# Performance work log

Hardware: AMD Instinct MI355X
Metric: run time of the kernel (lower is better)

## Reference

```python
import jax, jax.numpy as jnp
import numpy as np

N_NODES = 50000
N_EDGES = 800000
IN_DIM, HID, OUT = 512, 96, 64


def gcn_conv(x, W, b, src, dst, n_nodes):
    # PyG GCNConv: h = x W; aggregate with sym-normalized adjacency incl. self-loops; add bias.
    h = x @ W  # [N, out]
    ones = jnp.ones_like(dst, dtype=h.dtype)
    deg = jax.ops.segment_sum(ones, dst, num_segments=n_nodes) + 1.0  # +1 for self-loop
    dinv = jax.lax.rsqrt(deg)
    norm = dinv[src] * dinv[dst]  # [E]
    agg = jax.ops.segment_sum(h[src] * norm[:, None], dst, num_segments=n_nodes)
    agg = agg + h * (dinv * dinv)[:, None]  # self-loop messages
    return agg + b


def setup_inputs() -> dict:
    key = jax.random.key(0)
    ks = jax.random.split(key, 12)
    s = 0.05
    x = jax.random.normal(ks[0], (N_NODES, IN_DIM), jnp.float32)
    edge_index = jax.random.randint(ks[1], (2, N_EDGES), 0, N_NODES)
    return {
        "x": x,
        "edge_index": edge_index,
        "W0": jax.random.normal(ks[2], (IN_DIM, HID), jnp.float32) * s,
        "b0": jnp.zeros((HID,), jnp.float32),
        "W1": jax.random.normal(ks[3], (HID, HID), jnp.float32) * s,
        "b1": jnp.zeros((HID,), jnp.float32),
        "W2": jax.random.normal(ks[4], (HID, HID), jnp.float32) * s,
        "b2": jnp.zeros((HID,), jnp.float32),
        "fcW": jax.random.normal(ks[5], (HID, OUT), jnp.float32) * s,
        "fcb": jnp.zeros((OUT,), jnp.float32),
    }


def reference(x, edge_index, W0, b0, W1, b1, W2, b2, fcW, fcb):
    src, dst = edge_index[0], edge_index[1]
    n = x.shape[0]
    # eval mode: dropout is identity; bn=False so no batchnorm
    h = jax.nn.relu(gcn_conv(x, W0, b0, src, dst, n))
    h = jax.nn.relu(gcn_conv(h, W1, b1, src, dst, n))
    h = jax.nn.relu(gcn_conv(h, W2, b2, src, dst, n))
    out = h @ fcW + fcb
    return jnp.squeeze(out)
```

## Files before the change

kernel.cpp:

```cpp
#include <hip/hip_runtime.h>


constexpr int NN   = 50000;
constexpr int NE   = 800000;
constexpr int KIN  = 512;
constexpr int HIDD = 96;
constexpr int ODIM = 64;
constexpr int NBLK = (NN + 255) / 256;

typedef short bf16x8 __attribute__((ext_vector_type(8)));
typedef short s8v    __attribute__((ext_vector_type(8)));
typedef float f32x4  __attribute__((ext_vector_type(4)));
typedef _Float16 h8  __attribute__((ext_vector_type(8)));

__device__ inline short f2bf(float f) {
    union { float f; unsigned u; } v; v.f = f;
    unsigned r = v.u + 0x7FFFu + ((v.u >> 16) & 1u);
    return (short)(r >> 16);
}
__device__ inline short f2bf_trunc(float f) {
    union { float f; unsigned u; } v; v.f = f;
    return (short)(v.u >> 16);
}
__device__ inline float bf2f(short h) {
    union { unsigned u; float f; } v; v.u = ((unsigned)(unsigned short)h) << 16;
    return v.f;
}

__global__ void zero_int_kernel(int* __restrict__ p, int n) {
    int i = blockIdx.x * blockDim.x + threadIdx.x;
    if (i < n) p[i] = 0;
}

__global__ void hist_kernel(const int* __restrict__ dst, int* __restrict__ deg) {
    int e = blockIdx.x * blockDim.x + threadIdx.x;
    if (e < NE) atomicAdd(&deg[dst[e]], 1);
}

__global__ void scan1_kernel(const int* __restrict__ deg, int* __restrict__ excl,
                             int* __restrict__ partials) {
    __shared__ int tmp[256];
    const int tid = threadIdx.x;
    const int i = blockIdx.x * 256 + tid;
    const int v = (i < NN) ? deg[i] : 0;
    tmp[tid] = v;
    __syncthreads();
#pragma unroll
    for (int off = 1; off < 256; off <<= 1) {
        int t = (tid >= off) ? tmp[tid - off] : 0;
        __syncthreads();
        tmp[tid] += t;
        __syncthreads();
    }
    if (i < NN) excl[i] = tmp[tid] - v;
    if (tid == 255) partials[blockIdx.x] = tmp[tid];
}

__global__ void scan3_kernel(const int* __restrict__ excl, const int* __restrict__ partials,
                             const int* __restrict__ deg, int* __restrict__ rowstart,
                             float* __restrict__ dinv, int* __restrict__ cursor) {
    __shared__ int tmp[256];
    const int tid = threadIdx.x;
    tmp[tid] = (tid < (int)blockIdx.x) ? partials[tid] : 0;
    __syncthreads();
#pragma unroll
    for (int off = 128; off > 0; off >>= 1) {
        if (tid < off) tmp[tid] += tmp[tid + off];
        __syncthreads();
    }
    const int boff = tmp[0];
    const int i = blockIdx.x * 256 + tid;
    if (i < NN) {
        rowstart[i] = excl[i] + boff;
        dinv[i] = 1.0f / sqrtf((float)deg[i] + 1.0f);
        cursor[i] = 0;
    }
    if (blockIdx.x == 0 && tid == 0) rowstart[NN] = NE;
}

__global__ void scatter_kernel(const int* __restrict__ src, const int* __restrict__ dst,
                               const int* __restrict__ rowstart, int* __restrict__ cursor,
                               int* __restrict__ csr_src) {
    int e = blockIdx.x * blockDim.x + threadIdx.x;
    if (e < NE) {
        const int d = dst[e];
        const int pos = rowstart[d] + atomicAdd(&cursor[d], 1);
        csr_src[pos] = src[e];
    }
}

__global__ void pack_all(const float* __restrict__ W0, const float* __restrict__ W1,
                         const float* __restrict__ W2, const float* __restrict__ FC,
                         short* __restrict__ w0hi, short* __restrict__ w0lo,
                         short* __restrict__ w1hi, short* __restrict__ w1lo,
                         short* __restrict__ w2hi, short* __restrict__ w2lo,
                         short* __restrict__ fchi, short* __restrict__ fclo) {
    const int idx = blockIdx.x * 256 + threadIdx.x;
    const float* W; short *hi, *lo; int M, li;
    if      (idx < 49152) { W = W0; hi = w0hi; lo = w0lo; M = 96; li = idx; }
    else if (idx < 58368) { W = W1; hi = w1hi; lo = w1lo; M = 96; li = idx - 49152; }
    else if (idx < 67584) { W = W2; hi = w2hi; lo = w2lo; M = 96; li = idx - 58368; }
    else if (idx < 73728) { W = FC; hi = fchi; lo = fclo; M = 64; li = idx - 67584; }
    else return;
    const int CT = M >> 4;
    const int j = li & 7;
    const int lane = (li >> 3) & 63;
    const int t = li >> 9;
    const int ct = t % CT;
    const int kc = t / CT;
    const int k = kc * 32 + (lane >> 4) * 8 + j;
    const int n = ct * 16 + (lane & 15);
    const float w = W[k * M + n];
    const short h = f2bf(w);
    hi[li] = h;
    lo[li] = f2bf_trunc(w - bf2f(h));
}

template <int K>
__launch_bounds__(512, 6)
__global__ void mfma_gemm_f(const float* __restrict__ A, const short* __restrict__ Whi,
                            const short* __restrict__ Wlo, const float* __restrict__ dinv,
                            _Float16* __restrict__ C, int N) {
    constexpr int CT = 6;
    constexpr int KCH = K / 64;
    constexpr int PH  = KCH / 2;
    __shared__ short sHi[4 * 3072];
    __shared__ short sLo[4 * 3072];

    const int tid = threadIdx.x;
    const int lane = tid & 63;
    const int wave = tid >> 6;
    const int rw = wave & 3;
    const int kh = wave >> 2;
    const int q = lane >> 4;
    const int m = lane & 15;
    const int row = blockIdx.x * 64 + rw * 16 + m;
    const int arow = (row < N) ? row : (N - 1);

    f32x4 acc[CT];
#pragma unroll
    for (int c = 0; c < CT; ++c) acc[c] = f32x4{0.f, 0.f, 0.f, 0.f};

    const float* ap = A + (size_t)arow * K + kh * (K / 2) + q * 8;
    float4 a0 = *(const float4*)(ap);
    float4 a1 = *(const float4*)(ap + 4);

#pragma unroll
    for (int p = 0; p < PH; ++p) {
#pragma unroll
        for (int i = 0; i < 3; ++i) {
            const int ci = i * 512 + tid;
            const int slot = ci / 384;
            const int within = ci - slot * 384;
            const int kcg = (slot >> 1) * KCH + p * 2 + (slot & 1);
            const int so = kcg * 3072 + within * 8;
            const int doff = ci * 8;
            *(float4*)(sHi + doff) = *(const float4*)(Whi + so);
            *(float4*)(sLo + doff) = *(const float4*)(Wlo + so);
        }
        __syncthreads();

#pragma unroll
        for (int kc = 0; kc < 2; ++kc) {
            const float af[8] = {a0.x, a0.y, a0.z, a0.w, a1.x, a1.y, a1.z, a1.w};
            bf16x8 ahi, alo;
#pragma unroll
            for (int j = 0; j < 8; ++j) {
                const short h = f2bf(af[j]);
                ahi[j] = h;
                alo[j] = f2bf_trunc(af[j] - bf2f(h));
            }
            if (p * 2 + kc + 1 < KCH) {
                ap += 32;
                a0 = *(const float4*)(ap);
                a1 = *(const float4*)(ap + 4);
            }
            const int slot = kh * 2 + kc;
            const short* hbase = sHi + slot * 3072 + lane * 8;
            const short* lbase = sLo + slot * 3072 + lane * 8;
#pragma unroll
            for (int c = 0; c < CT; ++c) {
                const bf16x8 wh = *(const bf16x8*)(hbase + c * 512);
                const bf16x8 wl = *(const bf16x8*)(lbase + c * 512);
                acc[c] = __builtin_amdgcn_mfma_f32_16x16x32_bf16(ahi, wh, acc[c], 0, 0, 0);
                acc[c] = __builtin_amdgcn_mfma_f32_16x16x32_bf16(alo, wh, acc[c], 0, 0, 0);
                acc[c] = __builtin_amdgcn_mfma_f32_16x16x32_bf16(ahi, wl, acc[c], 0, 0, 0);
            }
        }
        __syncthreads();
    }

    float* sAcc = (float*)sHi;
    if (kh == 1) {
#pragma unroll
        for (int c = 0; c < CT; ++c)
            *(f32x4*)(sAcc + ((rw * 64 + lane) * CT + c) * 4) = acc[c];
    }
    __syncthreads();
    if (kh == 0) {
#pragma unroll
        for (int c = 0; c < CT; ++c) {
            const f32x4 o = *(const f32x4*)(sAcc + ((rw * 64 + lane) * CT + c) * 4);
            acc[c][0] += o[0]; acc[c][1] += o[1]; acc[c][2] += o[2]; acc[c][3] += o[3];
        }
        const int rbase = blockIdx.x * 64 + rw * 16 + q * 4;
#pragma unroll
        for (int r = 0; r < 4; ++r) {
            const int orow = rbase + r;
            if (orow < N) {
                const float s = dinv[orow];
#pragma unroll
                for (int c = 0; c < CT; ++c)
                    C[(size_t)orow * 96 + c * 16 + m] = (_Float16)(acc[c][r] * s);
            }
        }
    }
}

constexpr int APAD = 104;
template <int M, bool FC>
__launch_bounds__(768, 6)
__global__ void fused_gg(const int* __restrict__ rowstart, const float* __restrict__ dinv,
                         const int* __restrict__ csr_src, const _Float16* __restrict__ hs,
                         const float* __restrict__ gb,
                         const short* __restrict__ Whi, const short* __restrict__ Wlo,
                         const float* __restrict__ bias2,
                         _Float16* __restrict__ Ch, float* __restrict__ Cf, int N) {
    constexpr int CT = M / 16;
    __shared__ short sAhi[64 * APAD];
    __shared__ short sAlo[64 * APAD];

    const int tid = threadIdx.x;
    const int nb = blockIdx.x * 64;
    const int nl = tid / 12;
    const int fl = tid - nl * 12;
    const int node = nb + nl;

    s8v hi8, lo8;
    if (node < N) {
        const _Float16* __restrict__ hp = hs + fl * 8;
        float acc0[8], acc1[8];
        {
            const h8 sv = *(const h8*)(hp + (size_t)node * 96);
#pragma unroll
            for (int e = 0; e < 8; ++e) { acc0[e] = (float)sv[e]; acc1[e] = 0.f; }
        }
        int j = rowstart[node];
        const int jend = rowstart[node + 1];
        for (; j + 4 <= jend; j += 4) {
            const int s0 = csr_src[j], s1 = csr_src[j + 1];
            const int s2 = csr_src[j + 2], s3 = csr_src[j + 3];
            const h8 v0 = *(const h8*)(hp + (size_t)s0 * 96);
            const h8 v1 = *(const h8*)(hp + (size_t)s1 * 96);
            const h8 v2 = *(const h8*)(hp + (size_t)s2 * 96);
            const h8 v3 = *(const h8*)(hp + (size_t)s3 * 96);
#pragma unroll
            for (int e = 0; e < 8; ++e) {
                acc0[e] += (float)v0[e] + (float)v2[e];
                acc1[e] += (float)v1[e] + (float)v3[e];
            }
        }
        for (; j < jend; ++j) {
            const h8 v0 = *(const h8*)(hp + (size_t)csr_src[j] * 96);
#pragma unroll
            for (int e = 0; e < 8; ++e) acc0[e] += (float)v0[e];
        }
        const float di = dinv[node];
#pragma unroll
        for (int e = 0; e < 8; ++e) {
            const float o = fmaxf(fmaf(di, acc0[e] + acc1[e], gb[fl * 8 + e]), 0.0f);
            const short h = f2bf(o);
            hi8[e] = h;
            lo8[e] = f2bf_trunc(o - bf2f(h));
        }
    } else {
#pragma unroll
        for (int e = 0; e < 8; ++e) { hi8[e] = 0; lo8[e] = 0; }
    }
    *(s8v*)(sAhi + nl * APAD + fl * 8) = hi8;
    *(s8v*)(sAlo + nl * APAD + fl * 8) = lo8;
    __syncthreads();

    const int lane = tid & 63;
    const int wave = tid >> 6;
    const int rw = wave & 3;
    const int c0 = (wave >> 2) * 2;
    const int q = lane >> 4;
    const int m = lane & 15;

    if (c0 < CT) {
        bf16x8 Ah[3], Al[3];
#pragma unroll
        for (int kc = 0; kc < 3; ++kc) {
            const int off = (rw * 16 + m) * APAD + kc * 32 + q * 8;
            Ah[kc] = *(const bf16x8*)(sAhi + off);
            Al[kc] = *(const bf16x8*)(sAlo + off);
        }

        f32x4 gacc[2];
        gacc[0] = f32x4{0.f, 0.f, 0.f, 0.f};
        gacc[1] = f32x4{0.f, 0.f, 0.f, 0.f};

#pragma unroll
        for (int kc = 0; kc < 3; ++kc) {
#pragma unroll
            for (int c = 0; c < 2; ++c) {
                const int fo = ((kc * CT + c0 + c) * 64 + lane) * 8;
                const bf16x8 wh = *(const bf16x8*)(Whi + fo);
                const bf16x8 wl = *(const bf16x8*)(Wlo + fo);
                gacc[c] = __builtin_amdgcn_mfma_f32_16x16x32_bf16(Ah[kc], wh, gacc[c], 0, 0, 0);
                gacc[c] = __builtin_amdgcn_mfma_f32_16x16x32_bf16(Al[kc], wh, gacc[c], 0, 0, 0);
                gacc[c] = __builtin_amdgcn_mfma_f32_16x16x32_bf16(Ah[kc], wl, gacc[c], 0, 0, 0);
            }
        }

        const int rbase = nb + rw * 16 + q * 4;
#pragma unroll
        for (int r = 0; r < 4; ++r) {
            const int orow = rbase + r;
            if (orow < N) {
                if (FC) {
#pragma unroll
                    for (int c = 0; c < 2; ++c)
                        Cf[(size_t)orow * M + (c0 + c) * 16 + m] = gacc[c][r] + bias2[(c0 + c) * 16 + m];
                } else {
                    const float s = dinv[orow];
#pragma unroll
                    for (int c = 0; c < 2; ++c)
                        Ch[(size_t)orow * M + (c0 + c) * 16 + m] = (_Float16)(gacc[c][r] * s);
                }
            }
        }
    }
}

extern "C" void kernel_launch(void* const* d_in, const int* in_sizes, int n_in,
                              void* d_out, int out_size, void* d_ws, size_t ws_size,
                              hipStream_t stream) {
    const float* x   = (const float*)d_in[0];
    const int*   ei  = (const int*)d_in[1];
    const float* W0  = (const float*)d_in[2];
    const float* b0  = (const float*)d_in[3];
    const float* W1  = (const float*)d_in[4];
    const float* b1  = (const float*)d_in[5];
    const float* W2  = (const float*)d_in[6];
    const float* b2  = (const float*)d_in[7];
    const float* fcW = (const float*)d_in[8];
    const float* fcb = (const float*)d_in[9];
    float* out = (float*)d_out;

    const int* src = ei;
    const int* dst = ei + NE;

    float* ws = (float*)d_ws;
    float* dinv     = ws;
    int*   deg      = (int*)(ws + 50176);
    int*   excl     = (int*)(ws + 100352);
    int*   cursor   = (int*)(ws + 150528);
    int*   rowstart = (int*)(ws + 200704);
    int*   partials = (int*)(ws + 250880);
    int*   csr_src  = (int*)(ws + 251136);
    short* w0hi = (short*)(ws + 1051392);
    short* w0lo = (short*)(ws + 1075968);
    short* w1hi = (short*)(ws + 1100544);
    short* w1lo = (short*)(ws + 1105152);
    short* w2hi = (short*)(ws + 1109760);
    short* w2lo = (short*)(ws + 1114368);
    short* fchi = (short*)(ws + 1118976);
    short* fclo = (short*)(ws + 1122048);
    _Float16* hsA = (_Float16*)(ws + 1125120);
    _Float16* hsB = (_Float16*)(ws + 3525120);

    dim3 b256(256);
    const int gN = NBLK;
    const int gE = (NE + 255) / 256;
    const int gGem = (NN + 63) / 64;
    const int gPack = (73728 + 255) / 256;

    zero_int_kernel<<<gN, b256, 0, stream>>>(deg, NN);
    hist_kernel<<<gE, b256, 0, stream>>>(dst, deg);
    scan1_kernel<<<gN, b256, 0, stream>>>(deg, excl, partials);
    scan3_kernel<<<gN, b256, 0, stream>>>(excl, partials, deg, rowstart, dinv, cursor);
    scatter_kernel<<<gE, b256, 0, stream>>>(src, dst, rowstart, cursor, csr_src);
    pack_all<<<gPack, b256, 0, stream>>>(W0, W1, W2, fcW, w0hi, w0lo, w1hi, w1lo,
                                         w2hi, w2lo, fchi, fclo);

    mfma_gemm_f<KIN><<<gGem, dim3(512), 0, stream>>>(x, w0hi, w0lo, dinv, hsA, NN);

    fused_gg<HIDD, false><<<gGem, dim3(768), 0, stream>>>(
        rowstart, dinv, csr_src, hsA, b0, w1hi, w1lo, nullptr, hsB, nullptr, NN);

    fused_gg<HIDD, false><<<gGem, dim3(768), 0, stream>>>(
        rowstart, dinv, csr_src, hsB, b1, w2hi, w2lo, nullptr, hsA, nullptr, NN);

    fused_gg<ODIM, true><<<gGem, dim3(768), 0, stream>>>(
        rowstart, dinv, csr_src, hsA, b2, fchi, fclo, fcb, nullptr, out, NN);
}
```

Baseline: 375.7 us.

## Record edge rank in histogram, fuse zeroing with weight packing, unroll gather by eight

The histogram kernel now stores each edge's atomic return value as its rank, so the scatter kernel writes directly without a second pass of atomics on a cursor array. Cursor zeroing is gone, and deg zeroing is merged with weight packing into one launch, cutting one kernel launch. The CSR gather loop gains an 8-way unrolled body to keep more independent loads in flight. The cost is an extra 800K-int rank buffer write and read, plus more register pressure in the fused aggregation kernel.

```diff
diff --git a/kernel.cpp b/kernel.cpp
--- a/kernel.cpp
+++ b/kernel.cpp
@@ -27,75 +27,19 @@
     return v.f;
 }
 
-__global__ void zero_int_kernel(int* __restrict__ p, int n) {
-    int i = blockIdx.x * blockDim.x + threadIdx.x;
-    if (i < n) p[i] = 0;
-}
-
-__global__ void hist_kernel(const int* __restrict__ dst, int* __restrict__ deg) {
-    int e = blockIdx.x * blockDim.x + threadIdx.x;
-    if (e < NE) atomicAdd(&deg[dst[e]], 1);
-}
-
-__global__ void scan1_kernel(const int* __restrict__ deg, int* __restrict__ excl,
-                             int* __restrict__ partials) {
-    __shared__ int tmp[256];
-    const int tid = threadIdx.x;
-    const int i = blockIdx.x * 256 + tid;
-    const int v = (i < NN) ? deg[i] : 0;
-    tmp[tid] = v;
-    __syncthreads();
-#pragma unroll
-    for (int off = 1; off < 256; off <<= 1) {
-        int t = (tid >= off) ? tmp[tid - off] : 0;
-        __syncthreads();
-        tmp[tid] += t;
-        __syncthreads();
-    }
-    if (i < NN) excl[i] = tmp[tid] - v;
-    if (tid == 255) partials[blockIdx.x] = tmp[tid];
-}
-
-__global__ void scan3_kernel(const int* __restrict__ excl, const int* __restrict__ partials,
-                             const int* __restrict__ deg, int* __restrict__ rowstart,
-                             float* __restrict__ dinv, int* __restrict__ cursor) {
-    __shared__ int tmp[256];
-    const int tid = threadIdx.x;
-    tmp[tid] = (tid < (int)blockIdx.x) ? partials[tid] : 0;
-    __syncthreads();
-#pragma unroll
-    for (int off = 128; off > 0; off >>= 1) {
-        if (tid < off) tmp[tid] += tmp[tid + off];
-        __syncthreads();
-    }
-    const int boff = tmp[0];
-    const int i = blockIdx.x * 256 + tid;
-    if (i < NN) {
-        rowstart[i] = excl[i] + boff;
-        dinv[i] = 1.0f / sqrtf((float)deg[i] + 1.0f);
-        cursor[i] = 0;
-    }
-    if (blockIdx.x == 0 && tid == 0) rowstart[NN] = NE;
-}
-
-__global__ void scatter_kernel(const int* __restrict__ src, const int* __restrict__ dst,
-                               const int* __restrict__ rowstart, int* __restrict__ cursor,
-                               int* __restrict__ csr_src) {
-    int e = blockIdx.x * blockDim.x + threadIdx.x;
-    if (e < NE) {
-        const int d = dst[e];
-        const int pos = rowstart[d] + atomicAdd(&cursor[d], 1);
-        csr_src[pos] = src[e];
-    }
-}
-
-__global__ void pack_all(const float* __restrict__ W0, const float* __restrict__ W1,
-                         const float* __restrict__ W2, const float* __restrict__ FC,
-                         short* __restrict__ w0hi, short* __restrict__ w0lo,
-                         short* __restrict__ w1hi, short* __restrict__ w1lo,
-                         short* __restrict__ w2hi, short* __restrict__ w2lo,
-                         short* __restrict__ fchi, short* __restrict__ fclo) {
-    const int idx = blockIdx.x * 256 + threadIdx.x;
+__global__ void zero_pack(int* __restrict__ deg,
+                          const float* __restrict__ W0, const float* __restrict__ W1,
+                          const float* __restrict__ W2, const float* __restrict__ FC,
+                          short* __restrict__ w0hi, short* __restrict__ w0lo,
+                          short* __restrict__ w1hi, short* __restrict__ w1lo,
+                          short* __restrict__ w2hi, short* __restrict__ w2lo,
+                          short* __restrict__ fchi, short* __restrict__ fclo) {
+    if (blockIdx.x < NBLK) {
+        const int i = blockIdx.x * 256 + threadIdx.x;
+        if (i < NN) deg[i] = 0;
+        return;
+    }
+    const int idx = (blockIdx.x - NBLK) * 256 + threadIdx.x;
     const float* W; short *hi, *lo; int M, li;
     if      (idx < 49152) { W = W0; hi = w0hi; lo = w0lo; M = 96; li = idx; }
     else if (idx < 58368) { W = W1; hi = w1hi; lo = w1lo; M = 96; li = idx - 49152; }
@@ -116,6 +60,62 @@
     lo[li] = f2bf_trunc(w - bf2f(h));
 }
 
+__global__ void hist_kernel(const int* __restrict__ dst, int* __restrict__ deg,
+                            int* __restrict__ rank) {
+    int e = blockIdx.x * blockDim.x + threadIdx.x;
+    if (e < NE) rank[e] = atomicAdd(&deg[dst[e]], 1);
+}
+
+__global__ void scan1_kernel(const int* __restrict__ deg, int* __restrict__ excl,
+                             int* __restrict__ partials) {
+    __shared__ int tmp[256];
+    const int tid = threadIdx.x;
+    const int i = blockIdx.x * 256 + tid;
+    const int v = (i < NN) ? deg[i] : 0;
+    tmp[tid] = v;
+    __syncthreads();
+#pragma unroll
+    for (int off = 1; off < 256; off <<= 1) {
+        int t = (tid >= off) ? tmp[tid - off] : 0;
+        __syncthreads();
+        tmp[tid] += t;
+        __syncthreads();
+    }
+    if (i < NN) excl[i] = tmp[tid] - v;
+    if (tid == 255) partials[blockIdx.x] = tmp[tid];
+}
+
+__global__ void scan3_kernel(const int* __restrict__ excl, const int* __restrict__ partials,
+                             const int* __restrict__ deg, int* __restrict__ rowstart,
+                             float* __restrict__ dinv) {
+    __shared__ int tmp[256];
+    const int tid = threadIdx.x;
+    tmp[tid] = (tid < (int)blockIdx.x) ? partials[tid] : 0;
+    __syncthreads();
+#pragma unroll
+    for (int off = 128; off > 0; off >>= 1) {
+        if (tid < off) tmp[tid] += tmp[tid + off];
+        __syncthreads();
+    }
+    const int boff = tmp[0];
+    const int i = blockIdx.x * 256 + tid;
+    if (i < NN) {
+        rowstart[i] = excl[i] + boff;
+        dinv[i] = 1.0f / sqrtf((float)deg[i] + 1.0f);
+    }
+    if (blockIdx.x == 0 && tid == 0) rowstart[NN] = NE;
+}
+
+__global__ void scatter_kernel(const int* __restrict__ src, const int* __restrict__ dst,
+                               const int* __restrict__ rowstart, const int* __restrict__ rank,
+                               int* __restrict__ csr_src) {
+    int e = blockIdx.x * blockDim.x + threadIdx.x;
+    if (e < NE) {
+        const int d = dst[e];
+        csr_src[rowstart[d] + rank[e]] = src[e];
+    }
+}
+
 template <int K>
 __launch_bounds__(512, 6)
 __global__ void mfma_gemm_f(const float* __restrict__ A, const short* __restrict__ Whi,
@@ -247,6 +247,25 @@
         }
         int j = rowstart[node];
         const int jend = rowstart[node + 1];
+        for (; j + 8 <= jend; j += 8) {
+            const int s0 = csr_src[j],     s1 = csr_src[j + 1];
+            const int s2 = csr_src[j + 2], s3 = csr_src[j + 3];
+            const int s4 = csr_src[j + 4], s5 = csr_src[j + 5];
+            const int s6 = csr_src[j + 6], s7 = csr_src[j + 7];
+            const h8 v0 = *(const h8*)(hp + (size_t)s0 * 96);
+            const h8 v1 = *(const h8*)(hp + (size_t)s1 * 96);
+            const h8 v2 = *(const h8*)(hp + (size_t)s2 * 96);
+            const h8 v3 = *(const h8*)(hp + (size_t)s3 * 96);
+            const h8 v4 = *(const h8*)(hp + (size_t)s4 * 96);
+            const h8 v5 = *(const h8*)(hp + (size_t)s5 * 96);
+            const h8 v6 = *(const h8*)(hp + (size_t)s6 * 96);
+            const h8 v7 = *(const h8*)(hp + (size_t)s7 * 96);
+#pragma unroll
+            for (int e = 0; e < 8; ++e) {
+                acc0[e] += ((float)v0[e] + (float)v4[e]) + ((float)v2[e] + (float)v6[e]);
+                acc1[e] += ((float)v1[e] + (float)v5[e]) + ((float)v3[e] + (float)v7[e]);
+            }
+        }
         for (; j + 4 <= jend; j += 4) {
             const int s0 = csr_src[j], s1 = csr_src[j + 1];
             const int s2 = csr_src[j + 2], s3 = csr_src[j + 3];
@@ -356,7 +375,6 @@
     float* dinv     = ws;
     int*   deg      = (int*)(ws + 50176);
     int*   excl     = (int*)(ws + 100352);
-    int*   cursor   = (int*)(ws + 150528);
     int*   rowstart = (int*)(ws + 200704);
     int*   partials = (int*)(ws + 250880);
     int*   csr_src  = (int*)(ws + 251136);
@@ -370,20 +388,20 @@
     short* fclo = (short*)(ws + 1122048);
     _Float16* hsA = (_Float16*)(ws + 1125120);
     _Float16* hsB = (_Float16*)(ws + 3525120);
+    int*   rank    = (int*)(ws + 5925120);
 
     dim3 b256(256);
     const int gN = NBLK;
     const int gE = (NE + 255) / 256;
     const int gGem = (NN + 63) / 64;
-    const int gPack = (73728 + 255) / 256;
-
-    zero_int_kernel<<<gN, b256, 0, stream>>>(deg, NN);
-    hist_kernel<<<gE, b256, 0, stream>>>(dst, deg);
+    const int gZP = NBLK + (73728 + 255) / 256;
+
+    zero_pack<<<gZP, b256, 0, stream>>>(deg, W0, W1, W2, fcW, w0hi, w0lo, w1hi, w1lo,
+                                        w2hi, w2lo, fchi, fclo);
+    hist_kernel<<<gE, b256, 0, stream>>>(dst, deg, rank);
     scan1_kernel<<<gN, b256, 0, stream>>>(deg, excl, partials);
-    scan3_kernel<<<gN, b256, 0, stream>>>(excl, partials, deg, rowstart, dinv, cursor);
-    scatter_kernel<<<gE, b256, 0, stream>>>(src, dst, rowstart, cursor, csr_src);
-    pack_all<<<gPack, b256, 0, stream>>>(W0, W1, W2, fcW, w0hi, w0lo, w1hi, w1lo,
-                                         w2hi, w2lo, fchi, fclo);
+    scan3_kernel<<<gN, b256, 0, stream>>>(excl, partials, deg, rowstart, dinv);
+    scatter_kernel<<<gE, b256, 0, stream>>>(src, dst, rowstart, rank, csr_src);
 
     mfma_gemm_f<KIN><<<gGem, dim3(512), 0, stream>>>(x, w0hi, w0lo, dinv, hsA, NN);
 
```

After: 345.1 us. 8.1% less time.
